# Kernel tuning notes

Hardware: AMD Instinct MI355X
Metric: run time of the kernel (lower is better)

Reference implementation:

```python
import jax, jax.numpy as jnp
import numpy as np

B, F, D = 512, 128, 1024
EPS = 1e-5

def _ln(x, g, b):
    mu = jnp.mean(x, axis=-1, keepdims=True)
    var = jnp.mean(jnp.square(x - mu), axis=-1, keepdims=True)
    return (x - mu) * jax.lax.rsqrt(var + EPS) * g + b

def setup_inputs() -> dict:
    key = jax.random.key(0)
    ks = jax.random.split(key, 8)
    inp = {
        "text_embeds": jax.random.normal(ks[0], (B, D), jnp.float32),
        "video_embeds": jax.random.normal(ks[1], (B, F, D), jnp.float32),
    }
    # Linear weights: torch init is eye for all proj/linear layers; use small random
    # perturbation of identity to keep math non-trivial but realistic.
    def w(k):
        return jnp.eye(D, dtype=jnp.float32) + 0.02 * jax.random.normal(k, (D, D), jnp.float32)
    inp["q_w"], inp["k_w"], inp["v_w"] = w(ks[2]), w(ks[3]), w(ks[4])
    inp["out_w"], inp["lin_w"] = w(ks[5]), w(ks[6])
    for n in ("q_b", "k_b", "v_b", "out_b", "lin_b"):
        inp[n] = jnp.zeros((D,), jnp.float32)
    for i in (1, 2, 3):
        inp[f"ln{i}_g"] = jnp.ones((D,), jnp.float32)
        inp[f"ln{i}_b"] = jnp.zeros((D,), jnp.float32)
    return inp

def reference(text_embeds, video_embeds, q_w, k_w, v_w, out_w, lin_w,
              q_b, k_b, v_b, out_b, lin_b,
              ln1_g, ln1_b, ln2_g, ln2_b, ln3_g, ln3_b):
    t = _ln(text_embeds, ln1_g, ln1_b)                 # [B, D]
    vf = _ln(video_embeds, ln1_g, ln1_b)               # [B, F, D]
    q = t @ q_w.T + q_b                                # [B, D]
    k = vf @ k_w.T + k_b                               # [B, F, D]
    v = vf @ v_w.T + v_b                               # [B, F, D]
    logits = jnp.einsum("bd,bfd->bf", q, k) / jnp.sqrt(jnp.float32(D))
    w_att = jax.nn.softmax(logits, axis=-1)            # [B, F]
    attn = jnp.einsum("bf,bfd->bd", w_att, v)          # [B, D]
    attn = attn @ out_w.T + out_b
    attn_out = _ln(attn, ln2_g, ln2_b)
    linear_out = attn_out @ lin_w.T + lin_b
    # dropout: eval mode (identity)
    out = attn_out + linear_out
    return _ln(out, ln3_g, ln3_b)
```

## Files before the change

kernel.cpp:

```cpp
#include <hip/hip_runtime.h>

#define B_ 512
#define F_ 128
#define D_ 1024
#define EPS_ 1e-5f

typedef float f32x4 __attribute__((ext_vector_type(4)));
typedef __bf16 bf16x4 __attribute__((ext_vector_type(4)));
typedef __bf16 bf16x8 __attribute__((ext_vector_type(8)));

template <int OUT>
__global__ __launch_bounds__(256) void k_ln(
    const float* __restrict__ X, const float* __restrict__ g,
    const float* __restrict__ bv, float* __restrict__ Yf,
    __bf16* __restrict__ Yh, __bf16* __restrict__ Yl) {
  int row = blockIdx.x, t = threadIdx.x;
  f32x4 xv = *(const f32x4*)(X + (size_t)row * D_ + t * 4);
  float s = xv[0] + xv[1] + xv[2] + xv[3];
  float ss = xv[0] * xv[0] + xv[1] * xv[1] + xv[2] * xv[2] + xv[3] * xv[3];
#pragma unroll
  for (int o = 32; o > 0; o >>= 1) { s += __shfl_xor(s, o); ss += __shfl_xor(ss, o); }
  __shared__ float ws[4][2];
  int w = t >> 6;
  if ((t & 63) == 0) { ws[w][0] = s; ws[w][1] = ss; }
  __syncthreads();
  s = ws[0][0] + ws[1][0] + ws[2][0] + ws[3][0];
  ss = ws[0][1] + ws[1][1] + ws[2][1] + ws[3][1];
  float mu = s * (1.0f / D_);
  float var = ss * (1.0f / D_) - mu * mu;
  float rs = rsqrtf(var + EPS_);
  f32x4 gg = *(const f32x4*)(g + t * 4);
  f32x4 bb = *(const f32x4*)(bv + t * 4);
  f32x4 o4;
#pragma unroll
  for (int i = 0; i < 4; i++) o4[i] = (xv[i] - mu) * rs * gg[i] + bb[i];
  if (OUT == 0) {
    *(f32x4*)(Yf + (size_t)row * D_ + t * 4) = o4;
  } else {
    bf16x4 h4, l4;
#pragma unroll
    for (int i = 0; i < 4; i++) {
      h4[i] = (__bf16)o4[i];
      l4[i] = (__bf16)(o4[i] - (float)h4[i]);
    }
    *(bf16x4*)(Yh + (size_t)row * D_ + t * 4) = h4;
    *(bf16x4*)(Yl + (size_t)row * D_ + t * 4) = l4;
  }
}

__global__ __launch_bounds__(256) void k_final(
    const __bf16* __restrict__ X1h, const __bf16* __restrict__ X1l,
    const float* __restrict__ X2, const float* __restrict__ g,
    const float* __restrict__ bv, float* __restrict__ out) {
  int row = blockIdx.x, t = threadIdx.x;
  bf16x4 h4 = *(const bf16x4*)(X1h + (size_t)row * D_ + t * 4);
  bf16x4 l4 = *(const bf16x4*)(X1l + (size_t)row * D_ + t * 4);
  f32x4 b = *(const f32x4*)(X2 + (size_t)row * D_ + t * 4);
  f32x4 v;
#pragma unroll
  for (int i = 0; i < 4; i++) v[i] = (float)h4[i] + (float)l4[i] + b[i];
  float s = v[0] + v[1] + v[2] + v[3];
  float ss = v[0] * v[0] + v[1] * v[1] + v[2] * v[2] + v[3] * v[3];
#pragma unroll
  for (int o = 32; o > 0; o >>= 1) { s += __shfl_xor(s, o); ss += __shfl_xor(ss, o); }
  __shared__ float ws[4][2];
  int w = t >> 6;
  if ((t & 63) == 0) { ws[w][0] = s; ws[w][1] = ss; }
  __syncthreads();
  s = ws[0][0] + ws[1][0] + ws[2][0] + ws[3][0];
  ss = ws[0][1] + ws[1][1] + ws[2][1] + ws[3][1];
  float mu = s * (1.0f / D_);
  float var = ss * (1.0f / D_) - mu * mu;
  float rs = rsqrtf(var + EPS_);
  f32x4 gg = *(const f32x4*)(g + t * 4);
  f32x4 bb = *(const f32x4*)(bv + t * 4);
  f32x4 o4;
#pragma unroll
  for (int i = 0; i < 4; i++) o4[i] = (v[i] - mu) * rs * gg[i] + bb[i];
  *(f32x4*)(out + (size_t)row * D_ + t * 4) = o4;
}

__global__ __launch_bounds__(256) void k_wprep(
    const float* __restrict__ w0, const float* __restrict__ w1,
    const float* __restrict__ w2, const float* __restrict__ w3,
    const float* __restrict__ w4, __bf16* __restrict__ o0,
    __bf16* __restrict__ o1, __bf16* __restrict__ o2,
    __bf16* __restrict__ o3, __bf16* __restrict__ o4p) {
  int z = blockIdx.z;
  const float* src = (z == 0) ? w0 : (z == 1) ? w1 : (z == 2) ? w2 : (z == 3) ? w3 : w4;
  __bf16* dst = (z == 0) ? o0 : (z == 1) ? o1 : (z == 2) ? o2 : (z == 3) ? o3 : o4p;
  int t = threadIdx.x;
  if (z != 1) {
    int row = blockIdx.y * 32 + (t >> 3);
    int col = blockIdx.x * 32 + (t & 7) * 4;
    f32x4 v = *(const f32x4*)(src + (size_t)row * D_ + col);
    bf16x4 o;
    o[0] = (__bf16)v[0]; o[1] = (__bf16)v[1]; o[2] = (__bf16)v[2]; o[3] = (__bf16)v[3];
    *(bf16x4*)(dst + (size_t)row * D_ + col) = o;
  } else {
    __shared__ float tile[32][33];
    int ti = blockIdx.y, tj = blockIdx.x;
    int c = t & 31, r0 = t >> 5;
#pragma unroll
    for (int i = 0; i < 4; i++) {
      int r = r0 + i * 8;
      tile[r][c] = src[(size_t)(ti * 32 + r) * D_ + tj * 32 + c];
    }
    __syncthreads();
#pragma unroll
    for (int i = 0; i < 4; i++) {
      int r = r0 + i * 8;
      dst[(size_t)(tj * 32 + r) * D_ + ti * 32 + c] = (__bf16)tile[c][r];
    }
  }
}

template <int OUT>
__global__ __launch_bounds__(64) void k_gemm32(
    const __bf16* __restrict__ Ah, const __bf16* __restrict__ Al,
    const __bf16* __restrict__ W, const float* __restrict__ bias,
    float* __restrict__ Cf, __bf16* __restrict__ Ch, __bf16* __restrict__ Cl,
    int N, int K) {
  int lane = threadIdx.x;
  int r = lane & 15, quad = lane >> 4;
  int tn = blockIdx.x, tm = blockIdx.y;
  const __bf16* pah0 = Ah + (size_t)(tm * 32 + r) * K + quad * 8;
  const __bf16* pah1 = pah0 + (size_t)16 * K;
  const __bf16* pal0 = Al + (size_t)(tm * 32 + r) * K + quad * 8;
  const __bf16* pal1 = pal0 + (size_t)16 * K;
  const __bf16* pw0 = W + (size_t)(tn * 32 + r) * K + quad * 8;
  const __bf16* pw1 = pw0 + (size_t)16 * K;
  f32x4 acc00 = {0,0,0,0}, acc01 = {0,0,0,0}, acc10 = {0,0,0,0}, acc11 = {0,0,0,0};
  bf16x8 ah0 = *(const bf16x8*)pah0, ah1 = *(const bf16x8*)pah1;
  bf16x8 al0 = *(const bf16x8*)pal0, al1 = *(const bf16x8*)pal1;
  bf16x8 w0v = *(const bf16x8*)pw0, w1v = *(const bf16x8*)pw1;
  for (int k0 = 0; k0 < K; k0 += 32) {
    int kn = (k0 + 32 < K) ? (k0 + 32) : 0;
    bf16x8 nah0 = *(const bf16x8*)(pah0 + kn);
    bf16x8 nah1 = *(const bf16x8*)(pah1 + kn);
    bf16x8 nal0 = *(const bf16x8*)(pal0 + kn);
    bf16x8 nal1 = *(const bf16x8*)(pal1 + kn);
    bf16x8 nw0 = *(const bf16x8*)(pw0 + kn);
    bf16x8 nw1 = *(const bf16x8*)(pw1 + kn);
    acc00 = __builtin_amdgcn_mfma_f32_16x16x32_bf16(ah0, w0v, acc00, 0, 0, 0);
    acc01 = __builtin_amdgcn_mfma_f32_16x16x32_bf16(ah0, w1v, acc01, 0, 0, 0);
    acc10 = __builtin_amdgcn_mfma_f32_16x16x32_bf16(ah1, w0v, acc10, 0, 0, 0);
    acc11 = __builtin_amdgcn_mfma_f32_16x16x32_bf16(ah1, w1v, acc11, 0, 0, 0);
    acc00 = __builtin_amdgcn_mfma_f32_16x16x32_bf16(al0, w0v, acc00, 0, 0, 0);
    acc01 = __builtin_amdgcn_mfma_f32_16x16x32_bf16(al0, w1v, acc01, 0, 0, 0);
    acc10 = __builtin_amdgcn_mfma_f32_16x16x32_bf16(al1, w0v, acc10, 0, 0, 0);
    acc11 = __builtin_amdgcn_mfma_f32_16x16x32_bf16(al1, w1v, acc11, 0, 0, 0);
    ah0 = nah0; ah1 = nah1; al0 = nal0; al1 = nal1; w0v = nw0; w1v = nw1;
  }
  int col0 = tn * 32 + r, col1 = col0 + 16;
  float b0 = bias ? bias[col0] : 0.0f;
  float b1 = bias ? bias[col1] : 0.0f;
  int row0 = tm * 32 + quad * 4;
#pragma unroll
  for (int i = 0; i < 4; i++) {
    float v00 = acc00[i] + b0, v01 = acc01[i] + b1;
    float v10 = acc10[i] + b0, v11 = acc11[i] + b1;
    size_t o00 = (size_t)(row0 + i) * N + col0, o01 = (size_t)(row0 + i) * N + col1;
    size_t o10 = (size_t)(row0 + 16 + i) * N + col0, o11 = (size_t)(row0 + 16 + i) * N + col1;
    if (OUT == 0) {
      Cf[o00] = v00; Cf[o01] = v01; Cf[o10] = v10; Cf[o11] = v11;
    } else {
      __bf16 h;
      h = (__bf16)v00; Ch[o00] = h; Cl[o00] = (__bf16)(v00 - (float)h);
      h = (__bf16)v01; Ch[o01] = h; Cl[o01] = (__bf16)(v01 - (float)h);
      h = (__bf16)v10; Ch[o10] = h; Cl[o10] = (__bf16)(v10 - (float)h);
      h = (__bf16)v11; Ch[o11] = h; Cl[o11] = (__bf16)(v11 - (float)h);
    }
  }
}

__global__ __launch_bounds__(256) void k_prep_q(
    const float* __restrict__ q2, const __bf16* __restrict__ qh,
    const __bf16* __restrict__ ql, const float* __restrict__ g,
    const float* __restrict__ bv, const float* __restrict__ kb,
    float* __restrict__ gq, float* __restrict__ sum_gq,
    float* __restrict__ dot_bq, float* __restrict__ qkb) {
  int b = blockIdx.x, t = threadIdx.x;
  f32x4 q2v = *(const f32x4*)(q2 + (size_t)b * D_ + t * 4);
  bf16x4 h4 = *(const bf16x4*)(qh + (size_t)b * D_ + t * 4);
  bf16x4 l4 = *(const bf16x4*)(ql + (size_t)b * D_ + t * 4);
  f32x4 gg = *(const f32x4*)(g + t * 4);
  f32x4 bb = *(const f32x4*)(bv + t * 4);
  f32x4 kk = *(const f32x4*)(kb + t * 4);
  f32x4 gqv;
  float s1 = 0.f, s2 = 0.f, s3 = 0.f;
#pragma unroll
  for (int i = 0; i < 4; i++) {
    gqv[i] = gg[i] * q2v[i];
    s1 += gqv[i];
    s2 += bb[i] * q2v[i];
    s3 += kk[i] * ((float)h4[i] + (float)l4[i]);
  }
  *(f32x4*)(gq + (size_t)b * D_ + t * 4) = gqv;
#pragma unroll
  for (int o = 32; o > 0; o >>= 1) {
    s1 += __shfl_xor(s1, o); s2 += __shfl_xor(s2, o); s3 += __shfl_xor(s3, o);
  }
  __shared__ float ws[4][3];
  int w = t >> 6;
  if ((t & 63) == 0) { ws[w][0] = s1; ws[w][1] = s2; ws[w][2] = s3; }
  __syncthreads();
  if (t == 0) {
    sum_gq[b] = ws[0][0] + ws[1][0] + ws[2][0] + ws[3][0];
    dot_bq[b] = ws[0][1] + ws[1][1] + ws[2][1] + ws[3][1];
    qkb[b] = ws[0][2] + ws[1][2] + ws[2][2] + ws[3][2];
  }
}

#define XPAD 1032
__global__ __launch_bounds__(1024) void k_attn(
    const float* __restrict__ video, const float* __restrict__ gq,
    const float* __restrict__ sum_gq, const float* __restrict__ dot_bq,
    const float* __restrict__ qkb, const float* __restrict__ g,
    const float* __restrict__ bv, __bf16* __restrict__ ctxh,
    __bf16* __restrict__ ctxl) {
  __shared__ float X[32][XPAD];
  __shared__ float l_s[32], mu_s[32], rs_s[32], a_s[32];
  __shared__ float alpha_s, S_s, C_s;
  int b = blockIdx.x, t = threadIdx.x;
  int row = t >> 5, c = t & 31;
  const float* vbase = video + ((size_t)b * F_ + row) * D_ + c * 4;
  f32x4 gqr[8];
  const float* gp = gq + (size_t)b * D_ + c * 4;
#pragma unroll
  for (int i = 0; i < 8; i++) gqr[i] = *(const f32x4*)(gp + i * 128);
  float sgq = sum_gq[b], dbq = dot_bq[b], qk = qkb[b];
  f32x4 vr[8];
#pragma unroll
  for (int i = 0; i < 8; i++) vr[i] = *(const f32x4*)(vbase + i * 128);
  float O = 0.0f;
  float m_run = -1e30f, S = 0.0f, Cc = 0.0f;
  for (int T = 0; T < 4; T++) {
    float sx = 0.f, sxx = 0.f, sxg = 0.f;
#pragma unroll
    for (int i = 0; i < 8; i++) {
      f32x4 v = vr[i];
      sx += v[0] + v[1] + v[2] + v[3];
      sxx += v[0]*v[0] + v[1]*v[1] + v[2]*v[2] + v[3]*v[3];
      f32x4 gg = gqr[i];
      sxg += v[0]*gg[0] + v[1]*gg[1] + v[2]*gg[2] + v[3]*gg[3];
      *(f32x4*)(&X[row][c * 4 + i * 128]) = v;
    }
#pragma unroll
    for (int o = 16; o > 0; o >>= 1) {
      sx += __shfl_xor(sx, o);
      sxx += __shfl_xor(sxx, o);
      sxg += __shfl_xor(sxg, o);
    }
    if (c == 0) {
      float mu = sx * (1.0f / D_);
      float var = sxx * (1.0f / D_) - mu * mu;
      float rs = rsqrtf(var + EPS_);
      l_s[row] = (rs * (sxg - mu * sgq) + dbq + qk) * 0.03125f;
      mu_s[row] = mu; rs_s[row] = rs;
    }
    if (T < 3) {
      const float* nb = vbase + (size_t)(T + 1) * 32 * D_;
#pragma unroll
      for (int i = 0; i < 8; i++) vr[i] = *(const f32x4*)(nb + i * 128);
    }
    __syncthreads();
    if (t < 32) {
      float lf = l_s[t], mt = lf;
#pragma unroll
      for (int o = 16; o > 0; o >>= 1) mt = fmaxf(mt, __shfl_xor(mt, o));
      float m_new = fmaxf(m_run, mt);
      float alpha = __expf(m_run - m_new);
      float e = __expf(lf - m_new);
      float af = e * rs_s[t];
      a_s[t] = af;
      float se = e, sc = af * mu_s[t];
#pragma unroll
      for (int o = 16; o > 0; o >>= 1) {
        se += __shfl_xor(se, o);
        sc += __shfl_xor(sc, o);
      }
      S = S * alpha + se;
      Cc = Cc * alpha + sc;
      m_run = m_new;
      if (t == 0) { alpha_s = alpha; S_s = S; C_s = Cc; }
    }
    __syncthreads();
    float alpha = alpha_s;
    float acc = 0.0f;
#pragma unroll
    for (int fi = 0; fi < 32; fi++) acc += a_s[fi] * X[fi][t];
    O = O * alpha + acc;
    if (T < 3) __syncthreads();
  }
  float inv = 1.0f / S_s;
  float v = g[t] * ((O - C_s) * inv) + bv[t];
  __bf16 h = (__bf16)v;
  ctxh[(size_t)b * D_ + t] = h;
  ctxl[(size_t)b * D_ + t] = (__bf16)(v - (float)h);
}

extern "C" void kernel_launch(void* const* d_in, const int* in_sizes, int n_in,
                              void* d_out, int out_size, void* d_ws, size_t ws_size,
                              hipStream_t stream) {
  (void)in_sizes; (void)n_in; (void)out_size; (void)ws_size;
  const float* text = (const float*)d_in[0];
  const float* video = (const float*)d_in[1];
  const float* q_w = (const float*)d_in[2];
  const float* k_w = (const float*)d_in[3];
  const float* v_w = (const float*)d_in[4];
  const float* out_w = (const float*)d_in[5];
  const float* lin_w = (const float*)d_in[6];
  const float* q_b = (const float*)d_in[7];
  const float* k_b = (const float*)d_in[8];
  const float* v_b = (const float*)d_in[9];
  const float* out_b = (const float*)d_in[10];
  const float* lin_b = (const float*)d_in[11];
  const float* ln1_g = (const float*)d_in[12];
  const float* ln1_b = (const float*)d_in[13];
  const float* ln2_g = (const float*)d_in[14];
  const float* ln2_b = (const float*)d_in[15];
  const float* ln3_g = (const float*)d_in[16];
  const float* ln3_b = (const float*)d_in[17];
  float* out = (float*)d_out;

  const size_t BD = (size_t)B_ * D_;
  const size_t DD = (size_t)D_ * D_;
  float* f = (float*)d_ws;
  float* slotF1 = f;
  float* slotF2 = f + BD;
  float* sum_gq = f + 2 * BD;
  float* dot_bq = sum_gq + B_;
  float* qkb = sum_gq + 2 * B_;
  __bf16* P1h = (__bf16*)(sum_gq + 4 * B_);
  __bf16* P1l = P1h + BD;
  __bf16* P2h = P1h + 2 * BD;
  __bf16* P2l = P1h + 3 * BD;
  __bf16* P3h = P1h + 4 * BD;
  __bf16* P3l = P1h + 5 * BD;
  __bf16* Wq = P1h + 6 * BD;
  __bf16* WkT = Wq + DD;
  __bf16* Wv = Wq + 2 * DD;
  __bf16* Wo = Wq + 3 * DD;
  __bf16* Wl = Wq + 4 * DD;

  dim3 gemm_grid(D_ / 32, B_ / 32);

  k_wprep<<<dim3(32, 32, 5), 256, 0, stream>>>(q_w, k_w, v_w, out_w, lin_w,
                                               Wq, WkT, Wv, Wo, Wl);
  k_ln<1><<<B_, 256, 0, stream>>>(text, ln1_g, ln1_b, nullptr, P1h, P1l);
  k_gemm32<1><<<gemm_grid, 64, 0, stream>>>(P1h, P1l, Wq, q_b, nullptr, P2h, P2l, D_, D_);
  k_gemm32<0><<<gemm_grid, 64, 0, stream>>>(P2h, P2l, WkT, nullptr, slotF1, nullptr, nullptr, D_, D_);
  k_prep_q<<<B_, 256, 0, stream>>>(slotF1, P2h, P2l, ln1_g, ln1_b, k_b,
                                   slotF2, sum_gq, dot_bq, qkb);
  k_attn<<<B_, 1024, 0, stream>>>(video, slotF2, sum_gq, dot_bq, qkb,
                                  ln1_g, ln1_b, P1h, P1l);
  k_gemm32<1><<<gemm_grid, 64, 0, stream>>>(P1h, P1l, Wv, v_b, nullptr, P2h, P2l, D_, D_);
  k_gemm32<0><<<gemm_grid, 64, 0, stream>>>(P2h, P2l, Wo, out_b, slotF1, nullptr, nullptr, D_, D_);
  k_ln<1><<<B_, 256, 0, stream>>>(slotF1, ln2_g, ln2_b, nullptr, P3h, P3l);
  k_gemm32<0><<<gemm_grid, 64, 0, stream>>>(P3h, P3l, Wl, lin_b, slotF2, nullptr, nullptr, D_, D_);
  k_final<<<B_, 256, 0, stream>>>(P3h, P3l, slotF2, ln3_g, ln3_b, out);
}
```

Baseline: 522.2 us.

## Split GEMM K dimension across eight waves with shared-memory reduction

Each 32x32 GEMM tile block now uses eight wavefronts that each process one eighth of the K dimension. Partial accumulators are then summed through a padded shared-memory buffer before the bias and store. This raises per-block parallelism and shortens the serial K loop for the five small 512x1024x1024 GEMMs, which were latency-bound with a single wave per block. The cost is extra LDS traffic, a barrier, and a larger block that may limit occupancy.

```diff
diff --git a/kernel.cpp b/kernel.cpp
--- a/kernel.cpp
+++ b/kernel.cpp
@@ -116,26 +116,28 @@
 }
 
 template <int OUT>
-__global__ __launch_bounds__(64) void k_gemm32(
+__global__ __launch_bounds__(512) void k_gemm32(
     const __bf16* __restrict__ Ah, const __bf16* __restrict__ Al,
     const __bf16* __restrict__ W, const float* __restrict__ bias,
     float* __restrict__ Cf, __bf16* __restrict__ Ch, __bf16* __restrict__ Cl,
     int N, int K) {
-  int lane = threadIdx.x;
+  int t = threadIdx.x;
+  int lane = t & 63, wv = t >> 6;
   int r = lane & 15, quad = lane >> 4;
   int tn = blockIdx.x, tm = blockIdx.y;
-  const __bf16* pah0 = Ah + (size_t)(tm * 32 + r) * K + quad * 8;
+  int kw = K >> 3;
+  const __bf16* pah0 = Ah + (size_t)(tm * 32 + r) * K + wv * kw + quad * 8;
   const __bf16* pah1 = pah0 + (size_t)16 * K;
-  const __bf16* pal0 = Al + (size_t)(tm * 32 + r) * K + quad * 8;
+  const __bf16* pal0 = Al + (size_t)(tm * 32 + r) * K + wv * kw + quad * 8;
   const __bf16* pal1 = pal0 + (size_t)16 * K;
-  const __bf16* pw0 = W + (size_t)(tn * 32 + r) * K + quad * 8;
+  const __bf16* pw0 = W + (size_t)(tn * 32 + r) * K + wv * kw + quad * 8;
   const __bf16* pw1 = pw0 + (size_t)16 * K;
   f32x4 acc00 = {0,0,0,0}, acc01 = {0,0,0,0}, acc10 = {0,0,0,0}, acc11 = {0,0,0,0};
   bf16x8 ah0 = *(const bf16x8*)pah0, ah1 = *(const bf16x8*)pah1;
   bf16x8 al0 = *(const bf16x8*)pal0, al1 = *(const bf16x8*)pal1;
   bf16x8 w0v = *(const bf16x8*)pw0, w1v = *(const bf16x8*)pw1;
-  for (int k0 = 0; k0 < K; k0 += 32) {
-    int kn = (k0 + 32 < K) ? (k0 + 32) : 0;
+  for (int k0 = 0; k0 < kw; k0 += 32) {
+    int kn = (k0 + 32 < kw) ? (k0 + 32) : 0;
     bf16x8 nah0 = *(const bf16x8*)(pah0 + kn);
     bf16x8 nah1 = *(const bf16x8*)(pah1 + kn);
     bf16x8 nal0 = *(const bf16x8*)(pal0 + kn);
@@ -152,24 +154,30 @@
     acc11 = __builtin_amdgcn_mfma_f32_16x16x32_bf16(al1, w1v, acc11, 0, 0, 0);
     ah0 = nah0; ah1 = nah1; al0 = nal0; al1 = nal1; w0v = nw0; w1v = nw1;
   }
-  int col0 = tn * 32 + r, col1 = col0 + 16;
-  float b0 = bias ? bias[col0] : 0.0f;
-  float b1 = bias ? bias[col1] : 0.0f;
-  int row0 = tm * 32 + quad * 4;
-#pragma unroll
-  for (int i = 0; i < 4; i++) {
-    float v00 = acc00[i] + b0, v01 = acc01[i] + b1;
-    float v10 = acc10[i] + b0, v11 = acc11[i] + b1;
-    size_t o00 = (size_t)(row0 + i) * N + col0, o01 = (size_t)(row0 + i) * N + col1;
-    size_t o10 = (size_t)(row0 + 16 + i) * N + col0, o11 = (size_t)(row0 + 16 + i) * N + col1;
+  __shared__ float red[8][64][17];
+  *(f32x4*)(&red[wv][lane][0])  = acc00;
+  *(f32x4*)(&red[wv][lane][4])  = acc01;
+  *(f32x4*)(&red[wv][lane][8])  = acc10;
+  *(f32x4*)(&red[wv][lane][12]) = acc11;
+  __syncthreads();
+  int re = lane & 15, qe = lane >> 4;
+#pragma unroll
+  for (int u = 0; u < 2; u++) {
+    int j = (t >> 6) * 2 + u;
+    int a = j >> 2, i = j & 3;
+    float val = 0.0f;
+#pragma unroll
+    for (int ww = 0; ww < 8; ww++) val += red[ww][lane][j];
+    int row = tm * 32 + qe * 4 + i + ((a >> 1) << 4);
+    int col = tn * 32 + re + ((a & 1) << 4);
+    if (bias) val += bias[col];
+    size_t o = (size_t)row * N + col;
     if (OUT == 0) {
-      Cf[o00] = v00; Cf[o01] = v01; Cf[o10] = v10; Cf[o11] = v11;
+      Cf[o] = val;
     } else {
-      __bf16 h;
-      h = (__bf16)v00; Ch[o00] = h; Cl[o00] = (__bf16)(v00 - (float)h);
-      h = (__bf16)v01; Ch[o01] = h; Cl[o01] = (__bf16)(v01 - (float)h);
-      h = (__bf16)v10; Ch[o10] = h; Cl[o10] = (__bf16)(v10 - (float)h);
-      h = (__bf16)v11; Ch[o11] = h; Cl[o11] = (__bf16)(v11 - (float)h);
+      __bf16 h = (__bf16)val;
+      Ch[o] = h;
+      Cl[o] = (__bf16)(val - (float)h);
     }
   }
 }
@@ -349,15 +357,15 @@
   k_wprep<<<dim3(32, 32, 5), 256, 0, stream>>>(q_w, k_w, v_w, out_w, lin_w,
                                                Wq, WkT, Wv, Wo, Wl);
   k_ln<1><<<B_, 256, 0, stream>>>(text, ln1_g, ln1_b, nullptr, P1h, P1l);
-  k_gemm32<1><<<gemm_grid, 64, 0, stream>>>(P1h, P1l, Wq, q_b, nullptr, P2h, P2l, D_, D_);
-  k_gemm32<0><<<gemm_grid, 64, 0, stream>>>(P2h, P2l, WkT, nullptr, slotF1, nullptr, nullptr, D_, D_);
+  k_gemm32<1><<<gemm_grid, 512, 0, stream>>>(P1h, P1l, Wq, q_b, nullptr, P2h, P2l, D_, D_);
+  k_gemm32<0><<<gemm_grid, 512, 0, stream>>>(P2h, P2l, WkT, nullptr, slotF1, nullptr, nullptr, D_, D_);
   k_prep_q<<<B_, 256, 0, stream>>>(slotF1, P2h, P2l, ln1_g, ln1_b, k_b,
                                    slotF2, sum_gq, dot_bq, qkb);
   k_attn<<<B_, 1024, 0, stream>>>(video, slotF2, sum_gq, dot_bq, qkb,
                                   ln1_g, ln1_b, P1h, P1l);
-  k_gemm32<1><<<gemm_grid, 64, 0, stream>>>(P1h, P1l, Wv, v_b, nullptr, P2h, P2l, D_, D_);
-  k_gemm32<0><<<gemm_grid, 64, 0, stream>>>(P2h, P2l, Wo, out_b, slotF1, nullptr, nullptr, D_, D_);
+  k_gemm32<1><<<gemm_grid, 512, 0, stream>>>(P1h, P1l, Wv, v_b, nullptr, P2h, P2l, D_, D_);
+  k_gemm32<0><<<gemm_grid, 512, 0, stream>>>(P2h, P2l, Wo, out_b, slotF1, nullptr, nullptr, D_, D_);
   k_ln<1><<<B_, 256, 0, stream>>>(slotF1, ln2_g, ln2_b, nullptr, P3h, P3l);
-  k_gemm32<0><<<gemm_grid, 64, 0, stream>>>(P3h, P3l, Wl, lin_b, slotF2, nullptr, nullptr, D_, D_);
+  k_gemm32<0><<<gemm_grid, 512, 0, stream>>>(P3h, P3l, Wl, lin_b, slotF2, nullptr, nullptr, D_, D_);
   k_final<<<B_, 256, 0, stream>>>(P3h, P3l, slotF2, ln3_g, ln3_b, out);
 }
```

Result: faster. 505.3 us (-3.2%).
